# Optimization experiments

Hardware: AMD Instinct MI355X
Metric: run time of the kernel (lower is better)

The kernel has to match this reference:

```python
import jax, jax.numpy as jnp
import numpy as np

AUDIO_DIM, SEM_DIM, ATTN_DIM = 512, 768, 128


def setup_inputs() -> dict:
    key = jax.random.key(0)
    ks = jax.random.split(key, 12)
    B, T, T_sem = 8, 4096, 1024
    s = lambda d: 1.0 / np.sqrt(d)
    return {
        "x_ct": jax.random.normal(ks[0], (B, AUDIO_DIM, T), jnp.float32),
        "sem_btd": jax.random.normal(ks[1], (B, T_sem, SEM_DIM), jnp.float32),
        "ln_w": jnp.ones((AUDIO_DIM,), jnp.float32),
        "ln_b": jnp.zeros((AUDIO_DIM,), jnp.float32),
        "Wq": jax.random.normal(ks[2], (AUDIO_DIM, ATTN_DIM), jnp.float32) * s(AUDIO_DIM),
        "bq": jnp.zeros((ATTN_DIM,), jnp.float32),
        "Wk": jax.random.normal(ks[3], (SEM_DIM, ATTN_DIM), jnp.float32) * s(SEM_DIM),
        "bk": jnp.zeros((ATTN_DIM,), jnp.float32),
        "Wv": jax.random.normal(ks[4], (SEM_DIM, ATTN_DIM), jnp.float32) * s(SEM_DIM),
        "bv": jnp.zeros((ATTN_DIM,), jnp.float32),
        "Wo": jax.random.normal(ks[5], (ATTN_DIM, AUDIO_DIM), jnp.float32) * s(ATTN_DIM),
        "bo": jnp.zeros((AUDIO_DIM,), jnp.float32),
    }


def _layernorm(x, w, b, eps=1e-5):
    mu = jnp.mean(x, axis=-1, keepdims=True)
    var = jnp.mean(jnp.square(x - mu), axis=-1, keepdims=True)
    return (x - mu) * jax.lax.rsqrt(var + eps) * w + b


def reference(x_ct, sem_btd, ln_w, ln_b, Wq, bq, Wk, bk, Wv, bv, Wo, bo):
    # x_ct: [B, C, T] -> [B, T, C]
    x = jnp.swapaxes(x_ct, 1, 2)
    x = _layernorm(x, ln_w, ln_b)
    Q = x @ Wq + bq                      # [B, T, A]
    K = sem_btd @ Wk + bk                # [B, S, A]
    V = sem_btd @ Wv + bv                # [B, S, A]
    scale = ATTN_DIM ** -0.5
    attn = jnp.einsum("bta,bsa->bts", Q, K) * scale
    attn = jax.nn.softmax(attn, axis=-1)  # dropout: eval mode (identity)
    ctx = jnp.einsum("bts,bsa->bta", attn, V)
    delta = ctx @ Wo + bo                # [B, T, C]
    return jnp.swapaxes(delta, 1, 2)     # [B, C, T]
```

## Files before the change

### kernel.cpp

```cpp
#include <hip/hip_runtime.h>
#include <hip/hip_bf16.h>
#include <math.h>

#define BATCH 8
#define TDIM 4096
#define SDIM 1024
#define CDIM 512
#define DDIM 768
#define ADIM 128

typedef short s8v __attribute__((ext_vector_type(8)));
typedef float f4v __attribute__((ext_vector_type(4)));

__device__ __forceinline__ short f2bf(float f) {
    unsigned u = __float_as_uint(f);
    u += 0x7fffu + ((u >> 16) & 1u);
    return (short)(u >> 16);
}
__device__ __forceinline__ float bf2f(short s) {
    return __uint_as_float(((unsigned)(unsigned short)s) << 16);
}
__device__ __forceinline__ f4v mfma16(s8v a, s8v b, f4v c) {
    return __builtin_amdgcn_mfma_f32_16x16x32_bf16(a, b, c, 0, 0, 0);
}

__global__ __launch_bounds__(256) void prep_w(
    const float* __restrict__ Wq, const float* __restrict__ Wk,
    const float* __restrict__ Wv, const float* __restrict__ Wo,
    short* __restrict__ WqT, short* __restrict__ WkT,
    short* __restrict__ WvT, short* __restrict__ WoT)
{
    int gid = blockIdx.x * 256 + threadIdx.x;
    {
        int k = gid >> 7, n = gid & 127;
        WqT[n * 512 + k] = f2bf(Wq[gid]);
    }
    #pragma unroll
    for (int i = 0; i < 2; ++i) {
        int e = gid + i * 65536;
        if (e < 98304) {
            int k = e >> 7, n = e & 127;
            WkT[n * 768 + k] = f2bf(Wk[e]);
            WvT[n * 768 + k] = f2bf(Wv[e]);
        }
    }
    {
        int k = gid >> 9, c = gid & 511;
        WoT[c * 128 + k] = f2bf(Wo[gid]);
    }
}

__global__ __launch_bounds__(256) void kv_proj(
    const float* __restrict__ sem,
    const short* __restrict__ WkT, const float* __restrict__ bk,
    const short* __restrict__ WvT, const float* __restrict__ bv,
    short* __restrict__ Kb, short* __restrict__ Vb)
{
    __shared__ __align__(16) short sA[32 * 40];
    __shared__ __align__(16) short sW[2][128 * 40];
    const int tid = threadIdx.x, lane = tid & 63, wave = tid >> 6;
    const int ln15 = lane & 15, q = lane >> 4, kq = q * 8;
    const int r0 = blockIdx.x * 32;
    const int b = r0 >> 10, sbase = r0 & 1023;
    const int kv = wave >> 1;
    const int mh = wave & 1;
    const int m  = mh * 16 + ln15;

    f4v acc[8];
    #pragma unroll
    for (int j = 0; j < 8; ++j) acc[j] = (f4v)0.0f;

    const int srow = tid >> 3;
    const int sk4  = (tid & 7) * 4;

    for (int kc = 0; kc < DDIM / 32; ++kc) {
        __syncthreads();
        {
            float4 f = *(const float4*)&sem[(size_t)(r0 + srow) * DDIM + kc * 32 + sk4];
            uint2 pk;
            pk.x = (unsigned short)f2bf(f.x) | ((unsigned)(unsigned short)f2bf(f.y) << 16);
            pk.y = (unsigned short)f2bf(f.z) | ((unsigned)(unsigned short)f2bf(f.w) << 16);
            *(uint2*)&sA[srow * 40 + sk4] = pk;
        }
        #pragma unroll
        for (int i = 0; i < 2; ++i) {
            int idx8 = i * 256 + tid;
            int n = idx8 >> 2, k8 = (idx8 & 3) * 8;
            *(s8v*)&sW[0][n * 40 + k8] = *(const s8v*)&WkT[(size_t)n * 768 + kc * 32 + k8];
            *(s8v*)&sW[1][n * 40 + k8] = *(const s8v*)&WvT[(size_t)n * 768 + kc * 32 + k8];
        }
        __syncthreads();
        s8v a = *(const s8v*)&sA[m * 40 + kq];
        #pragma unroll
        for (int j = 0; j < 8; ++j) {
            s8v bb = *(const s8v*)&sW[kv][(j * 16 + ln15) * 40 + kq];
            acc[j] = mfma16(a, bb, acc[j]);
        }
    }
    const int s_in_b = sbase + mh * 16 + q * 4;
    if (kv == 0) {
        #pragma unroll
        for (int j = 0; j < 8; ++j) {
            int col = j * 16 + ln15;
            float bias = bk[col];
            #pragma unroll
            for (int r = 0; r < 4; ++r)
                Kb[((size_t)b * SDIM + s_in_b + r) * ADIM + col] = f2bf(acc[j][r] + bias);
        }
    } else {
        #pragma unroll
        for (int j = 0; j < 8; ++j) {
            int col = j * 16 + ln15;
            float bias = bv[col];
            uint2 pk;
            pk.x = (unsigned short)f2bf(acc[j][0] + bias) | ((unsigned)(unsigned short)f2bf(acc[j][1] + bias) << 16);
            pk.y = (unsigned short)f2bf(acc[j][2] + bias) | ((unsigned)(unsigned short)f2bf(acc[j][3] + bias) << 16);
            *(uint2*)&Vb[((size_t)b * ADIM + col) * SDIM + s_in_b] = pk;
        }
    }
}

__global__ __launch_bounds__(256) void ln_q(
    const float* __restrict__ x, const float* __restrict__ lnw, const float* __restrict__ lnb,
    const short* __restrict__ WqT, const float* __restrict__ bq, short* __restrict__ Qb)
{
    __shared__ __align__(16) short xt[32 * 512];
    __shared__ __align__(16) char  ubuf[128 * 72 * 2];
    __shared__ float smu[32], srs[32];
    short* sWq  = (short*)ubuf;
    float* red1 = (float*)ubuf;
    float* red2 = (float*)(ubuf + 4224);
    const int tid = threadIdx.x, lane = tid & 63, wave = tid >> 6;
    const int ln15 = lane & 15, q = lane >> 4, kq = q * 8;
    const int b = blockIdx.x >> 7;
    const int t0 = (blockIdx.x & 127) * 32;
    const float* xb = x + (size_t)b * CDIM * TDIM;

    const int tq = (tid & 7) * 4;
    const int g  = tid >> 3;
    float ps1[4] = {0.f,0.f,0.f,0.f}, ps2[4] = {0.f,0.f,0.f,0.f};
    #pragma unroll
    for (int i = 0; i < 16; ++i) {
        int c = i * 32 + g;
        float4 f = *(const float4*)&xb[(size_t)c * TDIM + t0 + tq];
        float vv[4] = { f.x, f.y, f.z, f.w };
        int kb = c >> 3, cl = c & 7;
        #pragma unroll
        for (int jj = 0; jj < 4; ++jj) {
            int t = tq + jj;
            ps1[jj] += vv[jj]; ps2[jj] += vv[jj] * vv[jj];
            xt[t * 512 + ((kb ^ ((t >> 2) & 7)) * 8) + cl] = f2bf(vv[jj]);
        }
    }
    #pragma unroll
    for (int jj = 0; jj < 4; ++jj) {
        red1[(tq + jj) * 33 + g] = ps1[jj];
        red2[(tq + jj) * 33 + g] = ps2[jj];
    }
    __syncthreads();
    if (tid < 32) {
        float s1 = 0.f, s2 = 0.f;
        #pragma unroll 8
        for (int gg = 0; gg < 32; ++gg) { s1 += red1[tid * 33 + gg]; s2 += red2[tid * 33 + gg]; }
        float mu = s1 * (1.f / 512.f);
        float var = s2 * (1.f / 512.f) - mu * mu;
        smu[tid] = mu; srs[tid] = rsqrtf(var + 1e-5f);
    }
    __syncthreads();
    {
        const int cb = tid & 63;
        const int c8 = cb * 8;
        float w8[8], b8[8];
        #pragma unroll
        for (int jj = 0; jj < 8; ++jj) { w8[jj] = lnw[c8 + jj]; b8[jj] = lnb[c8 + jj]; }
        #pragma unroll
        for (int i = 0; i < 8; ++i) {
            int t = i * 4 + (tid >> 6);
            float mu = smu[t], rs = srs[t];
            short* p = &xt[t * 512 + ((cb ^ ((t >> 2) & 7)) * 8)];
            s8v v = *(s8v*)p;
            #pragma unroll
            for (int jj = 0; jj < 8; ++jj)
                v[jj] = f2bf((bf2f(v[jj]) - mu) * rs * w8[jj] + b8[jj]);
            *(s8v*)p = v;
        }
    }
    f4v acc[4];
    #pragma unroll
    for (int j = 0; j < 4; ++j) acc[j] = (f4v)0.0f;
    const int mrow = (wave & 1) * 16 + ln15;
    const int jb = (wave >> 1) * 4;
    for (int kc = 0; kc < 8; ++kc) {
        __syncthreads();
        #pragma unroll
        for (int i = 0; i < 4; ++i) {
            int idx8 = i * 256 + tid;
            int n = idx8 >> 3, k8 = (idx8 & 7) * 8;
            *(s8v*)&sWq[n * 72 + k8] = *(const s8v*)&WqT[(size_t)n * 512 + kc * 64 + k8];
        }
        __syncthreads();
        #pragma unroll
        for (int kk = 0; kk < 2; ++kk) {
            int kb = kc * 8 + kk * 4 + q;
            s8v a = *(const s8v*)&xt[mrow * 512 + ((kb ^ ((mrow >> 2) & 7)) * 8)];
            #pragma unroll
            for (int j = 0; j < 4; ++j) {
                s8v bb = *(const s8v*)&sWq[((jb + j) * 16 + ln15) * 72 + kk * 32 + kq];
                acc[j] = mfma16(a, bb, acc[j]);
            }
        }
    }
    const float scale = 0.08838834764831845f;
    #pragma unroll
    for (int j = 0; j < 4; ++j) {
        int col = (jb + j) * 16 + ln15;
        float bias = bq[col];
        #pragma unroll
        for (int r = 0; r < 4; ++r) {
            int t = t0 + (wave & 1) * 16 + q * 4 + r;
            Qb[((size_t)b * TDIM + t) * ADIM + col] = f2bf((acc[j][r] + bias) * scale);
        }
    }
}

__global__ __launch_bounds__(256) void attn(
    const short* __restrict__ Qb, const short* __restrict__ Kb,
    const short* __restrict__ Vb, short* __restrict__ Cx)
{
    __shared__ __align__(16) short sK [2][64 * 128];
    __shared__ __align__(16) short sVT[2][128 * 64];
    __shared__ __align__(16) short sP [64 * 64];
    const int tid = threadIdx.x, lane = tid & 63, wave = tid >> 6;
    const int ln15 = lane & 15, q = lane >> 4, kq = q * 8;
    const int b = blockIdx.x >> 6;
    const int t0 = (blockIdx.x & 63) * 64;
    const int m = wave * 16 + ln15;

    const int krow = tid >> 4, kkb = tid & 15;
    const int varow = tid >> 3, vkb = tid & 7;

    s8v qf[4];
    {
        const short* qp = Qb + ((size_t)b * TDIM + t0 + m) * ADIM + kq;
        #pragma unroll
        for (int kc = 0; kc < 4; ++kc) qf[kc] = *(const s8v*)(qp + kc * 32);
    }
    s8v ones;
    #pragma unroll
    for (int j = 0; j < 8; ++j) ones[j] = (short)0x3F80;

    f4v accO[8]; f4v accL = (f4v)0.0f;
    #pragma unroll
    for (int j = 0; j < 8; ++j) accO[j] = (f4v)0.0f;

    const short* Kbase = Kb + (size_t)b * SDIM * ADIM;
    const short* Vbase = Vb + (size_t)b * ADIM * SDIM;
    s8v rk[4], rv[4];

    #pragma unroll
    for (int i = 0; i < 4; ++i) {
        rk[i] = *(const s8v*)(Kbase + (size_t)(i * 16 + krow) * ADIM + kkb * 8);
        rv[i] = *(const s8v*)(Vbase + (size_t)(i * 32 + varow) * SDIM + vkb * 8);
    }
    #pragma unroll
    for (int i = 0; i < 4; ++i) {
        int r = i * 16 + krow;
        *(s8v*)&sK[0][r * 128 + ((kkb ^ (r & 15)) * 8)] = rk[i];
        int a = i * 32 + varow;
        *(s8v*)&sVT[0][a * 64 + ((vkb ^ (a & 7)) * 8)] = rv[i];
    }
    __syncthreads();

    for (int sc = 0; sc < SDIM / 64; ++sc) {
        const int cur = sc & 1;
        if (sc < 15) {
            const int s0n = (sc + 1) * 64;
            #pragma unroll
            for (int i = 0; i < 4; ++i) {
                rk[i] = *(const s8v*)(Kbase + (size_t)(s0n + i * 16 + krow) * ADIM + kkb * 8);
                rv[i] = *(const s8v*)(Vbase + (size_t)(i * 32 + varow) * SDIM + s0n + vkb * 8);
            }
        }
        #pragma unroll
        for (int j = 0; j < 4; ++j) {
            f4v sacc = (f4v)0.0f;
            const int row = j * 16 + ln15;
            #pragma unroll
            for (int kc = 0; kc < 4; ++kc) {
                s8v bb = *(const s8v*)&sK[cur][row * 128 + (((kc * 4 + q) ^ (row & 15)) * 8)];
                sacc = mfma16(qf[kc], bb, sacc);
            }
            #pragma unroll
            for (int r = 0; r < 4; ++r) {
                float ev = __expf(sacc[r]);
                int prow = wave * 16 + q * 4 + r;
                int pcol = j * 16 + ln15;
                sP[prow * 64 + (((pcol >> 3) ^ (prow & 7)) * 8) + (pcol & 7)] = f2bf(ev);
            }
        }
        #pragma unroll
        for (int kc = 0; kc < 2; ++kc) {
            s8v pa = *(const s8v*)&sP[m * 64 + (((kc * 4 + q) ^ (m & 7)) * 8)];
            accL = mfma16(pa, ones, accL);
            #pragma unroll
            for (int j = 0; j < 8; ++j) {
                int a = j * 16 + ln15;
                s8v bb = *(const s8v*)&sVT[cur][a * 64 + (((kc * 4 + q) ^ (a & 7)) * 8)];
                accO[j] = mfma16(pa, bb, accO[j]);
            }
        }
        if (sc < 15) {
            #pragma unroll
            for (int i = 0; i < 4; ++i) {
                int r = i * 16 + krow;
                *(s8v*)&sK[cur ^ 1][r * 128 + ((kkb ^ (r & 15)) * 8)] = rk[i];
                int a = i * 32 + varow;
                *(s8v*)&sVT[cur ^ 1][a * 64 + ((vkb ^ (a & 7)) * 8)] = rv[i];
            }
        }
        __syncthreads();
    }
    #pragma unroll
    for (int r = 0; r < 4; ++r) {
        float rinv = 1.0f / accL[r];
        int t = t0 + wave * 16 + q * 4 + r;
        #pragma unroll
        for (int j = 0; j < 8; ++j) {
            int col = j * 16 + ln15;
            Cx[((size_t)b * TDIM + t) * ADIM + col] = f2bf(accO[j][r] * rinv);
        }
    }
}

__global__ __launch_bounds__(256) void out_proj(
    const short* __restrict__ Cx, const short* __restrict__ WoT,
    const float* __restrict__ bo, float* __restrict__ out)
{
    __shared__ __align__(16) short sCtx[64 * 136];
    __shared__ __align__(16) char  buf[128 * 136 * 2];
    short* sWoT = (short*)buf;
    float* outT = (float*)buf;
    const int tid = threadIdx.x, lane = tid & 63, wave = tid >> 6;
    const int ln15 = lane & 15, q = lane >> 4, kq = q * 8;
    const int b = blockIdx.x >> 8;
    const int rem = blockIdx.x & 255;
    const int t0 = (rem & 63) * 64;
    const int c0 = (rem >> 6) * 128;

    #pragma unroll
    for (int i = 0; i < 4; ++i) {
        int idx8 = i * 256 + tid;
        int row = idx8 >> 4, a8 = (idx8 & 15) * 8;
        *(s8v*)&sCtx[row * 136 + a8] = *(const s8v*)&Cx[((size_t)b * TDIM + t0 + row) * ADIM + a8];
    }
    #pragma unroll
    for (int i = 0; i < 8; ++i) {
        int idx8 = i * 256 + tid;
        int n = idx8 >> 4, k8 = (idx8 & 15) * 8;
        *(s8v*)&sWoT[n * 136 + k8] = *(const s8v*)&WoT[(size_t)(c0 + n) * ADIM + k8];
    }
    __syncthreads();
    f4v acc[8];
    #pragma unroll
    for (int j = 0; j < 8; ++j) acc[j] = (f4v)0.0f;
    const int m = wave * 16 + ln15;
    #pragma unroll
    for (int kc = 0; kc < 4; ++kc) {
        s8v a = *(const s8v*)&sCtx[m * 136 + kc * 32 + kq];
        #pragma unroll
        for (int j = 0; j < 8; ++j) {
            s8v bb = *(const s8v*)&sWoT[(j * 16 + ln15) * 136 + kc * 32 + kq];
            acc[j] = mfma16(a, bb, acc[j]);
        }
    }
    __syncthreads();
    #pragma unroll
    for (int j = 0; j < 8; ++j) {
        int cl = j * 16 + ln15;
        float bias = bo[c0 + cl];
        #pragma unroll
        for (int r = 0; r < 4; ++r) {
            int tl = wave * 16 + q * 4 + r;
            outT[cl * 68 + tl] = acc[j][r] + bias;
        }
    }
    __syncthreads();
    #pragma unroll
    for (int i = 0; i < 8; ++i) {
        int idx4 = i * 256 + tid;
        int c = idx4 >> 4, t4 = (idx4 & 15) * 4;
        float4 v = *(const float4*)&outT[c * 68 + t4];
        *(float4*)&out[((size_t)b * CDIM + c0 + c) * TDIM + t0 + t4] = v;
    }
}

extern "C" void kernel_launch(void* const* d_in, const int* in_sizes, int n_in,
                              void* d_out, int out_size, void* d_ws, size_t ws_size,
                              hipStream_t stream) {
    const float* x   = (const float*)d_in[0];
    const float* sem = (const float*)d_in[1];
    const float* lnw = (const float*)d_in[2];
    const float* lnb = (const float*)d_in[3];
    const float* Wq  = (const float*)d_in[4];
    const float* bq  = (const float*)d_in[5];
    const float* Wk  = (const float*)d_in[6];
    const float* bk  = (const float*)d_in[7];
    const float* Wv  = (const float*)d_in[8];
    const float* bv  = (const float*)d_in[9];
    const float* Wo  = (const float*)d_in[10];
    const float* bo  = (const float*)d_in[11];
    float* out = (float*)d_out;

    short* ws  = (short*)d_ws;
    short* Qb  = ws;
    short* Kb  = Qb  + (size_t)BATCH * TDIM * ADIM;
    short* Vb  = Kb  + (size_t)BATCH * SDIM * ADIM;
    short* Cx  = Vb  + (size_t)BATCH * SDIM * ADIM;
    short* WqT = Cx  + (size_t)BATCH * TDIM * ADIM;
    short* WkT = WqT + 128 * 512;
    short* WvT = WkT + 128 * 768;
    short* WoT = WvT + 128 * 768;

    hipLaunchKernelGGL(prep_w,  dim3(256),  dim3(256), 0, stream, Wq, Wk, Wv, Wo, WqT, WkT, WvT, WoT);
    hipLaunchKernelGGL(kv_proj, dim3(256),  dim3(256), 0, stream, sem, WkT, bk, WvT, bv, Kb, Vb);
    hipLaunchKernelGGL(ln_q,    dim3(1024), dim3(256), 0, stream, x, lnw, lnb, WqT, bq, Qb);
    hipLaunchKernelGGL(attn,    dim3(512),  dim3(256), 0, stream, Qb, Kb, Vb, Cx);
    hipLaunchKernelGGL(out_proj,dim3(2048), dim3(256), 0, stream, Cx, WoT, bo, out);
}
```

Baseline: 234.9 us.

## Fold LayerNorm affine into Wq and apply normalization after the Q GEMM

LayerNorm gamma is folded into the bf16 Wq during weight prep, and two per-column vectors (beta·Wq and gamma·Wq) are precomputed with atomics. ln_q no longer runs a separate normalize pass over the shared-memory tile. It runs the GEMM on raw bf16 x and applies rstd*acc + u - mu*rstd*v in the epilogue. The x load is regrouped to write packed 4-channel bf16 words, and Wq tiles are register-prefetched one k-chunk ahead with padded LDS rows. The cost is an extra memset and atomic reduction, plus some accuracy risk because mean subtraction now happens after bf16 rounding of the unnormalized x.

```diff
diff --git a/kernel.cpp b/kernel.cpp
--- a/kernel.cpp
+++ b/kernel.cpp
@@ -27,13 +27,16 @@
 __global__ __launch_bounds__(256) void prep_w(
     const float* __restrict__ Wq, const float* __restrict__ Wk,
     const float* __restrict__ Wv, const float* __restrict__ Wo,
+    const float* __restrict__ lnw, const float* __restrict__ lnb,
     short* __restrict__ WqT, short* __restrict__ WkT,
-    short* __restrict__ WvT, short* __restrict__ WoT)
+    short* __restrict__ WvT, short* __restrict__ WoT,
+    float* __restrict__ uv)
 {
-    int gid = blockIdx.x * 256 + threadIdx.x;
+    int tid = threadIdx.x;
+    int gid = blockIdx.x * 256 + tid;
     {
         int k = gid >> 7, n = gid & 127;
-        WqT[n * 512 + k] = f2bf(Wq[gid]);
+        WqT[n * 512 + k] = f2bf(Wq[gid] * lnw[k]);
     }
     #pragma unroll
     for (int i = 0; i < 2; ++i) {
@@ -47,6 +50,19 @@
     {
         int k = gid >> 9, c = gid & 511;
         WoT[c * 128 + k] = f2bf(Wo[gid]);
+    }
+    if (blockIdx.x < 32) {
+        int a = tid & 127, half = tid >> 7;
+        float pu = 0.f, pv = 0.f;
+        #pragma unroll
+        for (int cc = 0; cc < 8; ++cc) {
+            int c = blockIdx.x * 16 + half * 8 + cc;
+            float wq = Wq[c * 128 + a];
+            pu += lnb[c] * wq;
+            pv += lnw[c] * wq;
+        }
+        atomicAdd(&uv[a], pu);
+        atomicAdd(&uv[128 + a], pv);
     }
 }
 
@@ -121,11 +137,14 @@
 }
 
 __global__ __launch_bounds__(256) void ln_q(
-    const float* __restrict__ x, const float* __restrict__ lnw, const float* __restrict__ lnb,
-    const short* __restrict__ WqT, const float* __restrict__ bq, short* __restrict__ Qb)
+    const float* __restrict__ x,
+    const short* __restrict__ WqT,
+    const float* __restrict__ bq,
+    const float* __restrict__ uv,
+    short* __restrict__ Qb)
 {
     __shared__ __align__(16) short xt[32 * 512];
-    __shared__ __align__(16) char  ubuf[128 * 72 * 2];
+    __shared__ __align__(16) char  ubuf[128 * 76 * 2];
     __shared__ float smu[32], srs[32];
     short* sWq  = (short*)ubuf;
     float* red1 = (float*)ubuf;
@@ -136,26 +155,37 @@
     const int t0 = (blockIdx.x & 127) * 32;
     const float* xb = x + (size_t)b * CDIM * TDIM;
 
-    const int tq = (tid & 7) * 4;
-    const int g  = tid >> 3;
+    const int tq  = (tid & 7) * 4;
+    const int cb  = tid >> 3;
+    const int rot = tid & 7;
     float ps1[4] = {0.f,0.f,0.f,0.f}, ps2[4] = {0.f,0.f,0.f,0.f};
     #pragma unroll
-    for (int i = 0; i < 16; ++i) {
-        int c = i * 32 + g;
-        float4 f = *(const float4*)&xb[(size_t)c * TDIM + t0 + tq];
-        float vv[4] = { f.x, f.y, f.z, f.w };
-        int kb = c >> 3, cl = c & 7;
+    for (int i = 0; i < 4; ++i) {
+        float4 f[4];
+        #pragma unroll
+        for (int jc = 0; jc < 4; ++jc)
+            f[jc] = *(const float4*)&xb[(size_t)(i * 128 + cb * 4 + jc) * TDIM + t0 + tq];
+        const int c4 = i * 128 + cb * 4;
+        const int blockX = ((c4 >> 3) ^ rot);
+        const int offs = c4 & 7;
         #pragma unroll
         for (int jj = 0; jj < 4; ++jj) {
-            int t = tq + jj;
-            ps1[jj] += vv[jj]; ps2[jj] += vv[jj] * vv[jj];
-            xt[t * 512 + ((kb ^ ((t >> 2) & 7)) * 8) + cl] = f2bf(vv[jj]);
+            float v0 = ((const float*)&f[0])[jj];
+            float v1 = ((const float*)&f[1])[jj];
+            float v2 = ((const float*)&f[2])[jj];
+            float v3 = ((const float*)&f[3])[jj];
+            ps1[jj] += (v0 + v1) + (v2 + v3);
+            ps2[jj] += (v0*v0 + v1*v1) + (v2*v2 + v3*v3);
+            uint2 pk;
+            pk.x = (unsigned short)f2bf(v0) | ((unsigned)(unsigned short)f2bf(v1) << 16);
+            pk.y = (unsigned short)f2bf(v2) | ((unsigned)(unsigned short)f2bf(v3) << 16);
+            *(uint2*)&xt[(tq + jj) * 512 + blockX * 8 + offs] = pk;
         }
     }
     #pragma unroll
     for (int jj = 0; jj < 4; ++jj) {
-        red1[(tq + jj) * 33 + g] = ps1[jj];
-        red2[(tq + jj) * 33 + g] = ps2[jj];
+        red1[(tq + jj) * 33 + cb] = ps1[jj];
+        red2[(tq + jj) * 33 + cb] = ps2[jj];
     }
     __syncthreads();
     if (tid < 32) {
@@ -166,46 +196,41 @@
         float var = s2 * (1.f / 512.f) - mu * mu;
         smu[tid] = mu; srs[tid] = rsqrtf(var + 1e-5f);
     }
-    __syncthreads();
-    {
-        const int cb = tid & 63;
-        const int c8 = cb * 8;
-        float w8[8], b8[8];
-        #pragma unroll
-        for (int jj = 0; jj < 8; ++jj) { w8[jj] = lnw[c8 + jj]; b8[jj] = lnb[c8 + jj]; }
-        #pragma unroll
-        for (int i = 0; i < 8; ++i) {
-            int t = i * 4 + (tid >> 6);
-            float mu = smu[t], rs = srs[t];
-            short* p = &xt[t * 512 + ((cb ^ ((t >> 2) & 7)) * 8)];
-            s8v v = *(s8v*)p;
-            #pragma unroll
-            for (int jj = 0; jj < 8; ++jj)
-                v[jj] = f2bf((bf2f(v[jj]) - mu) * rs * w8[jj] + b8[jj]);
-            *(s8v*)p = v;
-        }
-    }
+
     f4v acc[4];
     #pragma unroll
     for (int j = 0; j < 4; ++j) acc[j] = (f4v)0.0f;
     const int mrow = (wave & 1) * 16 + ln15;
     const int jb = (wave >> 1) * 4;
+    const int mr_rot = (mrow >> 2) & 7;
+    s8v wreg[4];
+    #pragma unroll
+    for (int i = 0; i < 4; ++i) {
+        int idx8 = i * 256 + tid;
+        wreg[i] = *(const s8v*)&WqT[(size_t)(idx8 >> 3) * 512 + (idx8 & 7) * 8];
+    }
     for (int kc = 0; kc < 8; ++kc) {
         __syncthreads();
         #pragma unroll
         for (int i = 0; i < 4; ++i) {
             int idx8 = i * 256 + tid;
-            int n = idx8 >> 3, k8 = (idx8 & 7) * 8;
-            *(s8v*)&sWq[n * 72 + k8] = *(const s8v*)&WqT[(size_t)n * 512 + kc * 64 + k8];
+            *(s8v*)&sWq[(idx8 >> 3) * 76 + (idx8 & 7) * 8] = wreg[i];
+        }
+        if (kc < 7) {
+            #pragma unroll
+            for (int i = 0; i < 4; ++i) {
+                int idx8 = i * 256 + tid;
+                wreg[i] = *(const s8v*)&WqT[(size_t)(idx8 >> 3) * 512 + (kc + 1) * 64 + (idx8 & 7) * 8];
+            }
         }
         __syncthreads();
         #pragma unroll
         for (int kk = 0; kk < 2; ++kk) {
             int kb = kc * 8 + kk * 4 + q;
-            s8v a = *(const s8v*)&xt[mrow * 512 + ((kb ^ ((mrow >> 2) & 7)) * 8)];
+            s8v a = *(const s8v*)&xt[mrow * 512 + ((kb ^ mr_rot) << 3)];
             #pragma unroll
             for (int j = 0; j < 4; ++j) {
-                s8v bb = *(const s8v*)&sWq[((jb + j) * 16 + ln15) * 72 + kk * 32 + kq];
+                s8v bb = *(const s8v*)&sWq[((jb + j) * 16 + ln15) * 76 + kk * 32 + kq];
                 acc[j] = mfma16(a, bb, acc[j]);
             }
         }
@@ -214,11 +239,13 @@
     #pragma unroll
     for (int j = 0; j < 4; ++j) {
         int col = (jb + j) * 16 + ln15;
-        float bias = bq[col];
+        float uu = uv[col] + bq[col];
+        float vv = uv[128 + col];
         #pragma unroll
         for (int r = 0; r < 4; ++r) {
-            int t = t0 + (wave & 1) * 16 + q * 4 + r;
-            Qb[((size_t)b * TDIM + t) * ADIM + col] = f2bf((acc[j][r] + bias) * scale);
+            int tl = (wave & 1) * 16 + q * 4 + r;
+            float qv = srs[tl] * acc[j][r] + uu - smu[tl] * srs[tl] * vv;
+            Qb[((size_t)b * TDIM + t0 + tl) * ADIM + col] = f2bf(qv * scale);
         }
     }
 }
@@ -420,10 +447,13 @@
     short* WkT = WqT + 128 * 512;
     short* WvT = WkT + 128 * 768;
     short* WoT = WvT + 128 * 768;
-
-    hipLaunchKernelGGL(prep_w,  dim3(256),  dim3(256), 0, stream, Wq, Wk, Wv, Wo, WqT, WkT, WvT, WoT);
+    float* uv  = (float*)(WoT + 512 * 128);
+
+    hipMemsetAsync(uv, 0, 256 * sizeof(float), stream);
+    hipLaunchKernelGGL(prep_w,  dim3(256),  dim3(256), 0, stream,
+                       Wq, Wk, Wv, Wo, lnw, lnb, WqT, WkT, WvT, WoT, uv);
     hipLaunchKernelGGL(kv_proj, dim3(256),  dim3(256), 0, stream, sem, WkT, bk, WvT, bv, Kb, Vb);
-    hipLaunchKernelGGL(ln_q,    dim3(1024), dim3(256), 0, stream, x, lnw, lnb, WqT, bq, Qb);
+    hipLaunchKernelGGL(ln_q,    dim3(1024), dim3(256), 0, stream, x, WqT, bq, uv, Qb);
     hipLaunchKernelGGL(attn,    dim3(512),  dim3(256), 0, stream, Qb, Kb, Vb, Cx);
     hipLaunchKernelGGL(out_proj,dim3(2048), dim3(256), 0, stream, Cx, WoT, bo, out);
 }
```

New measurement: 259.0 us. +10.2%, slower.
